# Optimization experiments

Measured on AMD Instinct MI355X. Metric: run time of the kernel, lower is better.

The kernel has to match this reference:

```python
import jax, jax.numpy as jnp
import numpy as np

N_NODES = 100000
N_EDGES = 1600000
IN_CH = 128
OUT_CH = 64
HID = 2 * OUT_CH  # 128


def setup_inputs() -> dict:
    key = jax.random.key(0)
    ks = jax.random.split(key, 8)
    s = lambda fan_in: 1.0 / np.sqrt(fan_in)
    return {
        "x": jax.random.normal(ks[0], (N_NODES, IN_CH), jnp.float32),
        "edge_index": jax.random.randint(ks[1], (2, N_EDGES), 0, N_NODES, dtype=jnp.int32),
        "W1": jax.random.normal(ks[2], (IN_CH, HID), jnp.float32) * s(IN_CH),
        "b1": jnp.zeros((HID,), jnp.float32),
        "W2": jax.random.normal(ks[3], (HID, HID), jnp.float32) * s(HID),
        "b2": jnp.zeros((HID,), jnp.float32),
        "W3": jax.random.normal(ks[4], (HID, OUT_CH), jnp.float32) * s(HID),
        "b3": jnp.zeros((OUT_CH,), jnp.float32),
    }


def reference(x, edge_index, W1, b1, W2, b2, W3, b3):
    N = x.shape[0]
    # GCNConv (PyG semantics): add self-loops, symmetric deg^{-1/2} normalization,
    # linear transform, scatter-add aggregation at destination, then bias.
    loops = jnp.arange(N, dtype=edge_index.dtype)
    src = jnp.concatenate([edge_index[0], loops])  # [E+N]
    dst = jnp.concatenate([edge_index[1], loops])  # [E+N]
    deg = jnp.zeros((N,), x.dtype).at[dst].add(1.0)  # in-degree incl. self-loop
    dinv = jnp.where(deg > 0, jax.lax.rsqrt(deg), 0.0)
    norm = (dinv[src] * dinv[dst])[:, None]  # [E+N, 1]

    def gcn_conv(h, W, b):
        h = h @ W  # transform first (smaller when out < in)
        msg = h[src] * norm  # gather + normalize, [E+N, C]
        agg = jnp.zeros((N, h.shape[1]), h.dtype).at[dst].add(msg)  # scatter-add
        return agg + b

    h = jax.nn.relu(gcn_conv(x, W1, b1))
    h = jax.nn.relu(gcn_conv(h, W2, b2))
    h = gcn_conv(h, W3, b3)
    return jnp.min(h, axis=0)  # min-pool over nodes -> [OUT_CH]
```

## Files before the change

kernel.cpp:

```cpp
#include <hip/hip_runtime.h>
#include <stdint.h>
#include <stddef.h>
#include <float.h>

typedef short bf16x8 __attribute__((ext_vector_type(8)));
typedef float f32x4 __attribute__((ext_vector_type(4)));

static __device__ __forceinline__ unsigned enc_min(float v) {
  unsigned u = __float_as_uint(v);
  return (u & 0x80000000u) ? ~u : (u | 0x80000000u);
}
static __device__ __forceinline__ unsigned short f2bf(float f) {
  unsigned u = __float_as_uint(f);
  u += 0x7fffu + ((u >> 16) & 1u);
  return (unsigned short)(u >> 16);
}
static __device__ __forceinline__ float bf2f(unsigned short b) {
  return __uint_as_float(((unsigned)b) << 16);
}
static __device__ __forceinline__ void acc8(float* a, uint4 v) {
  a[0] += __uint_as_float(v.x << 16);
  a[1] += __uint_as_float(v.x & 0xffff0000u);
  a[2] += __uint_as_float(v.y << 16);
  a[3] += __uint_as_float(v.y & 0xffff0000u);
  a[4] += __uint_as_float(v.z << 16);
  a[5] += __uint_as_float(v.z & 0xffff0000u);
  a[6] += __uint_as_float(v.w << 16);
  a[7] += __uint_as_float(v.w & 0xffff0000u);
}

__global__ __launch_bounds__(256) void k_count_bin(const int* __restrict__ edge, int E, int N,
                                                   int* __restrict__ cnt8,
                                                   int* __restrict__ bin_cur,
                                                   int2* __restrict__ pairs,
                                                   int binw, int bcap) {
  __shared__ int h[8], gbase[8], lfill[8];
  int cslot = blockIdx.x & 7;
  int* cnt = cnt8 + (size_t)cslot * N;
  int tid = threadIdx.x;
  int nt = (E + 1023) >> 10;
  for (int t = blockIdx.x; t < nt; t += gridDim.x) {
    int e0 = t << 10;
    if (tid < 8) { h[tid] = 0; lfill[tid] = 0; }
    __syncthreads();
    int d[4], s[4], g[4], r[4];
#pragma unroll
    for (int k = 0; k < 4; ++k) {
      int e = e0 + tid + k * 256;
      d[k] = -1;
      if (e < E) {
        d[k] = edge[E + e];
        s[k] = edge[e];
        g[k] = (int)((unsigned)d[k] / (unsigned)binw);
        r[k] = atomicAdd(&cnt[d[k]], 1);
        atomicAdd(&h[g[k]], 1);
      }
    }
    __syncthreads();
    if (tid < 8) gbase[tid] = atomicAdd(&bin_cur[tid], h[tid]);
    __syncthreads();
#pragma unroll
    for (int k = 0; k < 4; ++k) {
      if (d[k] >= 0) {
        int rr = atomicAdd(&lfill[g[k]], 1);
        int p = gbase[g[k]] + rr;
        unsigned packed = (unsigned)d[k] | ((unsigned)cslot << 17) | ((unsigned)r[k] << 20);
        if (p < bcap) pairs[(size_t)g[k] * bcap + p] = make_int2((int)packed, s[k]);
      }
    }
    __syncthreads();
  }
}

__global__ void k_scan1(const int* __restrict__ cnt8, int N,
                        int* __restrict__ cnt, int* __restrict__ incl,
                        int* __restrict__ bsum) {
  __shared__ int sm[1024];
  int tid = threadIdx.x;
  int i = blockIdx.x * 1024 + tid;
  int v = 0;
  if (i < N) {
#pragma unroll
    for (int g = 0; g < 8; ++g) v += cnt8[(size_t)g * N + i];
    cnt[i] = v;
  }
  sm[tid] = v;
  __syncthreads();
  for (int off = 1; off < 1024; off <<= 1) {
    int t = (tid >= off) ? sm[tid - off] : 0;
    __syncthreads();
    sm[tid] += t;
    __syncthreads();
  }
  if (i < N) incl[i] = sm[tid];
  if (tid == 1023) bsum[blockIdx.x] = sm[1023];
}

__global__ void k_scan2(const int* __restrict__ bsum, int nb, int* __restrict__ boff) {
  __shared__ int sm[128];
  int tid = threadIdx.x;
  int v = (tid < nb) ? bsum[tid] : 0;
  sm[tid] = v;
  __syncthreads();
  for (int off = 1; off < 128; off <<= 1) {
    int t = (tid >= off) ? sm[tid - off] : 0;
    __syncthreads();
    sm[tid] += t;
    __syncthreads();
  }
  if (tid < nb) boff[tid] = sm[tid] - v;
}

__global__ void k_aux(const int* __restrict__ cnt, const int* __restrict__ cnt8,
                      const int* __restrict__ incl, const int* __restrict__ boff,
                      int N, int E, int* __restrict__ row_ptr,
                      int* __restrict__ base8, float* __restrict__ dinv) {
  int i = blockIdx.x * blockDim.x + threadIdx.x;
  if (i < N) {
    int rp = incl[i] - cnt[i] + boff[i >> 10];
    row_ptr[i] = rp;
    dinv[i] = 1.0f / sqrtf((float)(cnt[i] + 1));
    int run = rp;
#pragma unroll
    for (int c = 0; c < 8; ++c) {
      base8[(size_t)c * N + i] = run;
      run += cnt8[(size_t)c * N + i];
    }
  } else if (i == N) {
    row_ptr[N] = E;
  }
}

__global__ void k_prepw(const float* __restrict__ W1, const float* __restrict__ W2,
                        const float* __restrict__ W3,
                        unsigned short* __restrict__ w1h, unsigned short* __restrict__ w1l,
                        unsigned short* __restrict__ w2h, unsigned short* __restrict__ w2l,
                        unsigned short* __restrict__ w3h, unsigned short* __restrict__ w3l) {
  const int K = 128;
  int idx = blockIdx.x * 256 + threadIdx.x;
  const float* W;
  unsigned short *oh, *ol;
  int Nn, base;
  if (idx < 16384) { W = W1; Nn = 128; oh = w1h; ol = w1l; base = idx; }
  else if (idx < 32768) { W = W2; Nn = 128; oh = w2h; ol = w2l; base = idx - 16384; }
  else if (idx < 40960) { W = W3; Nn = 64; oh = w3h; ol = w3l; base = idx - 32768; }
  else return;
  int n = base / K, k = base % K;
  float w = W[(size_t)k * Nn + n];
  unsigned short h = f2bf(w);
  unsigned short l = f2bf(w - bf2f(h));
  int nf = n >> 4, mloc = n & 15, kci = k >> 5, quad = (k >> 3) & 3, j = k & 7;
  size_t o = ((size_t)((nf * 4 + kci) * 64 + quad * 16 + mloc)) * 8 + j;
  oh[o] = h;
  ol[o] = l;
}

template <int NFW>
static __device__ __forceinline__ void gemm_body(const float* __restrict__ A,
                                                 const unsigned short* __restrict__ Wfh,
                                                 const unsigned short* __restrict__ Wfl,
                                                 const float* __restrict__ dinv,
                                                 unsigned short* __restrict__ P, int M,
                                                 int blk) {
  const int K = 128;
  const int COUT = NFW * 64;
  __shared__ unsigned short Ah[64][136];
  __shared__ unsigned short Al[64][136];
  int tid = threadIdx.x;
  int m0 = blk * 64;
  int w = tid >> 6, lane = tid & 63;

  bf16x8 bh[NFW][4], bl[NFW][4];
#pragma unroll
  for (int i = 0; i < NFW; ++i)
#pragma unroll
    for (int kci = 0; kci < 4; ++kci) {
      size_t o = ((size_t)(((w * NFW + i) * 4 + kci) * 64 + lane)) * 8;
      bh[i][kci] = *(const bf16x8*)&Wfh[o];
      bl[i][kci] = *(const bf16x8*)&Wfl[o];
    }

#pragma unroll
  for (int q = 0; q < 8; ++q) {
    int f = q * 256 + tid;
    int m = f >> 5, k4 = f & 31;
    int row = m0 + m;
    if (row >= M) row = M - 1;
    float4 v = *(const float4*)&A[(size_t)row * K + k4 * 4];
    unsigned short h0 = f2bf(v.x), h1 = f2bf(v.y), h2 = f2bf(v.z), h3 = f2bf(v.w);
    unsigned short l0 = f2bf(v.x - bf2f(h0)), l1 = f2bf(v.y - bf2f(h1));
    unsigned short l2 = f2bf(v.z - bf2f(h2)), l3 = f2bf(v.w - bf2f(h3));
    uint2 hh, ll;
    hh.x = (unsigned)h0 | ((unsigned)h1 << 16);
    hh.y = (unsigned)h2 | ((unsigned)h3 << 16);
    ll.x = (unsigned)l0 | ((unsigned)l1 << 16);
    ll.y = (unsigned)l2 | ((unsigned)l3 << 16);
    *(uint2*)&Ah[m][k4 * 4] = hh;
    *(uint2*)&Al[m][k4 * 4] = ll;
  }
  __syncthreads();

  int mloc = lane & 15, quad = lane >> 4;
  f32x4 acc[4][NFW];
#pragma unroll
  for (int rt = 0; rt < 4; ++rt)
#pragma unroll
    for (int i = 0; i < NFW; ++i) acc[rt][i] = (f32x4){0.f, 0.f, 0.f, 0.f};

#pragma unroll
  for (int rt = 0; rt < 4; ++rt) {
    const unsigned short* ph = &Ah[rt * 16 + mloc][quad * 8];
    const unsigned short* pl = &Al[rt * 16 + mloc][quad * 8];
#pragma unroll
    for (int kci = 0; kci < 4; ++kci) {
      bf16x8 ah = *(const bf16x8*)(ph + kci * 32);
      bf16x8 al = *(const bf16x8*)(pl + kci * 32);
#pragma unroll
      for (int i = 0; i < NFW; ++i) {
        acc[rt][i] = __builtin_amdgcn_mfma_f32_16x16x32_bf16(al, bh[i][kci], acc[rt][i], 0, 0, 0);
        acc[rt][i] = __builtin_amdgcn_mfma_f32_16x16x32_bf16(ah, bl[i][kci], acc[rt][i], 0, 0, 0);
        acc[rt][i] = __builtin_amdgcn_mfma_f32_16x16x32_bf16(ah, bh[i][kci], acc[rt][i], 0, 0, 0);
      }
    }
  }

#pragma unroll
  for (int rt = 0; rt < 4; ++rt) {
    int rbase = m0 + rt * 16 + quad * 4;
#pragma unroll
    for (int r = 0; r < 4; ++r) {
      int row = rbase + r;
      if (row < M) {
        float dv = dinv[row];
#pragma unroll
        for (int i = 0; i < NFW; ++i) {
          int nf = w * NFW + i;
          P[(size_t)row * COUT + nf * 16 + mloc] = f2bf(acc[rt][i][r] * dv);
        }
      }
    }
  }
}

__global__ __launch_bounds__(256) void k_fill_gemm(const float* __restrict__ A,
                                                   const unsigned short* __restrict__ Wfh,
                                                   const unsigned short* __restrict__ Wfl,
                                                   const float* __restrict__ dinv,
                                                   unsigned short* __restrict__ P, int M,
                                                   const int2* __restrict__ pairs,
                                                   const int* __restrict__ bin_cur, int bcap,
                                                   const int* __restrict__ base8, int N,
                                                   int* __restrict__ srcs, int ns) {
  if ((int)blockIdx.x >= ns) {
    gemm_body<2>(A, Wfh, Wfl, dinv, P, M, blockIdx.x - ns);
  } else {
    int grp = blockIdx.x & 7;
    int bslot = blockIdx.x >> 3;
    int nslot = ns >> 3;
    int cnt_g = bin_cur[grp];
    if (cnt_g > bcap) cnt_g = bcap;
    const int2* pp = pairs + (size_t)grp * bcap;
    for (int i = bslot * blockDim.x + threadIdx.x; i < cnt_g; i += nslot * blockDim.x) {
      int2 pr = pp[i];
      unsigned w = (unsigned)pr.x;
      int d = (int)(w & 0x1FFFFu);
      int c = (int)((w >> 17) & 7u);
      int r = (int)(w >> 20);
      srcs[base8[(size_t)c * N + d] + r] = pr.y;
    }
  }
}

template <int NFW>
__global__ __launch_bounds__(256) void k_agg_gemm(const unsigned short* __restrict__ Pin,
                                                  const int* __restrict__ row_ptr,
                                                  const int* __restrict__ srcs,
                                                  const float* __restrict__ dinv,
                                                  const float* __restrict__ bias,
                                                  const unsigned short* __restrict__ Wfh,
                                                  const unsigned short* __restrict__ Wfl,
                                                  unsigned short* __restrict__ Pout, int N) {
  const int COUT = NFW * 64;
  __shared__ unsigned short Ah[16][136];
  __shared__ unsigned short Al[16][136];
  int tid = threadIdx.x;
  int wv = tid >> 6, lane = tid & 63;
  int grp = lane >> 4, sub = lane & 15;
  int m = wv * 4 + grp;
  int d = blockIdx.x * 16 + m;
  int dc = d < N ? d : N - 1;
  bool valid = d < N;
  unsigned soff = (unsigned)sub * 16u;
  const char* Pb = (const char*)Pin;

  float a[8] = {0.f, 0.f, 0.f, 0.f, 0.f, 0.f, 0.f, 0.f};
  {
    uint4 v = *(const uint4*)(Pb + ((unsigned)dc * 256u + soff));
    acc8(a, v);
  }
  int lo = row_ptr[dc];
  int hi = row_ptr[valid ? d + 1 : dc];
  int j = lo;
  for (; j + 4 <= hi; j += 4) {
    unsigned i0 = (unsigned)srcs[j];
    unsigned i1 = (unsigned)srcs[j + 1];
    unsigned i2 = (unsigned)srcs[j + 2];
    unsigned i3 = (unsigned)srcs[j + 3];
    uint4 v0 = *(const uint4*)(Pb + (i0 * 256u + soff));
    uint4 v1 = *(const uint4*)(Pb + (i1 * 256u + soff));
    uint4 v2 = *(const uint4*)(Pb + (i2 * 256u + soff));
    uint4 v3 = *(const uint4*)(Pb + (i3 * 256u + soff));
    acc8(a, v0);
    acc8(a, v1);
    acc8(a, v2);
    acc8(a, v3);
  }
  for (; j < hi; ++j) {
    unsigned i0 = (unsigned)srcs[j];
    uint4 v0 = *(const uint4*)(Pb + (i0 * 256u + soff));
    acc8(a, v0);
  }

  bf16x8 bh[NFW][4], bl[NFW][4];
#pragma unroll
  for (int i = 0; i < NFW; ++i)
#pragma unroll
    for (int kci = 0; kci < 4; ++kci) {
      size_t o = ((size_t)(((wv * NFW + i) * 4 + kci) * 64 + lane)) * 8;
      bh[i][kci] = *(const bf16x8*)&Wfh[o];
      bl[i][kci] = *(const bf16x8*)&Wfl[o];
    }

  float dv = dinv[dc];
  int ch0 = sub * 8;
  float4 bv0 = *(const float4*)&bias[ch0];
  float4 bv1 = *(const float4*)&bias[ch0 + 4];
  float h[8];
  h[0] = dv * a[0] + bv0.x; h[1] = dv * a[1] + bv0.y;
  h[2] = dv * a[2] + bv0.z; h[3] = dv * a[3] + bv0.w;
  h[4] = dv * a[4] + bv1.x; h[5] = dv * a[5] + bv1.y;
  h[6] = dv * a[6] + bv1.z; h[7] = dv * a[7] + bv1.w;
#pragma unroll
  for (int k = 0; k < 8; ++k) h[k] = fmaxf(h[k], 0.f);
  unsigned short hb[8], lb[8];
#pragma unroll
  for (int k = 0; k < 8; ++k) {
    hb[k] = f2bf(h[k]);
    lb[k] = f2bf(h[k] - bf2f(hb[k]));
  }
  uint4 HH, LL;
  HH.x = (unsigned)hb[0] | ((unsigned)hb[1] << 16);
  HH.y = (unsigned)hb[2] | ((unsigned)hb[3] << 16);
  HH.z = (unsigned)hb[4] | ((unsigned)hb[5] << 16);
  HH.w = (unsigned)hb[6] | ((unsigned)hb[7] << 16);
  LL.x = (unsigned)lb[0] | ((unsigned)lb[1] << 16);
  LL.y = (unsigned)lb[2] | ((unsigned)lb[3] << 16);
  LL.z = (unsigned)lb[4] | ((unsigned)lb[5] << 16);
  LL.w = (unsigned)lb[6] | ((unsigned)lb[7] << 16);
  *(uint4*)&Ah[m][ch0] = HH;
  *(uint4*)&Al[m][ch0] = LL;
  __syncthreads();

  int mloc = lane & 15, quad = lane >> 4;
  f32x4 acc[NFW];
#pragma unroll
  for (int i = 0; i < NFW; ++i) acc[i] = (f32x4){0.f, 0.f, 0.f, 0.f};
#pragma unroll
  for (int kci = 0; kci < 4; ++kci) {
    bf16x8 ah = *(const bf16x8*)&Ah[mloc][quad * 8 + kci * 32];
    bf16x8 al = *(const bf16x8*)&Al[mloc][quad * 8 + kci * 32];
#pragma unroll
    for (int i = 0; i < NFW; ++i) {
      acc[i] = __builtin_amdgcn_mfma_f32_16x16x32_bf16(al, bh[i][kci], acc[i], 0, 0, 0);
      acc[i] = __builtin_amdgcn_mfma_f32_16x16x32_bf16(ah, bl[i][kci], acc[i], 0, 0, 0);
      acc[i] = __builtin_amdgcn_mfma_f32_16x16x32_bf16(ah, bh[i][kci], acc[i], 0, 0, 0);
    }
  }
  int rbase = blockIdx.x * 16 + quad * 4;
#pragma unroll
  for (int r = 0; r < 4; ++r) {
    int row = rbase + r;
    if (row < N) {
      float dvr = dinv[row];
#pragma unroll
      for (int i = 0; i < NFW; ++i) {
        int nf = wv * NFW + i;
        Pout[(size_t)row * COUT + nf * 16 + mloc] = f2bf(acc[i][r] * dvr);
      }
    }
  }
}

__global__ __launch_bounds__(256) void k_agg_pool(const unsigned short* __restrict__ P,
                                                  const int* __restrict__ row_ptr,
                                                  const int* __restrict__ srcs,
                                                  const float* __restrict__ dinv,
                                                  const float* __restrict__ bias,
                                                  unsigned* __restrict__ minenc, int N) {
  const int CAP = 448;
  __shared__ int s_idx[4][CAP];
  __shared__ float s_red[4][32];
  int tid = threadIdx.x;
  int wv = tid >> 6, lane = tid & 63;
  int b8 = blockIdx.x & 7;
  int slice = b8 >> 2, part = b8 & 3;
  int g0 = ((blockIdx.x >> 3) * 4 + part) * 64 + wv * 16;
  const char* Pb = (const char*)P + slice * 64;

  int i = lane >> 2, q = lane & 3;
  unsigned qoff = (unsigned)q * 16u;
  int d = g0 + i;
  int dc = d < N ? d : N - 1;
  bool valid = d < N;

  int e0 = row_ptr[g0 < N ? g0 : N];
  int e1 = row_ptr[(g0 + 16) < N ? (g0 + 16) : N];
  int lo_n = row_ptr[dc];
  int hi_n = row_ptr[valid ? d + 1 : dc];

  float a[8];
  {
    uint4 v = *(const uint4*)(Pb + ((unsigned)dc * 128u + qoff));
    a[0] = __uint_as_float(v.x << 16);
    a[1] = __uint_as_float(v.x & 0xffff0000u);
    a[2] = __uint_as_float(v.y << 16);
    a[3] = __uint_as_float(v.y & 0xffff0000u);
    a[4] = __uint_as_float(v.z << 16);
    a[5] = __uint_as_float(v.z & 0xffff0000u);
    a[6] = __uint_as_float(v.w << 16);
    a[7] = __uint_as_float(v.w & 0xffff0000u);
  }

  for (int w0 = e0; w0 < e1; w0 += CAP) {
    int wend = min(w0 + CAP, e1);
    int cnt = wend - w0;
    __builtin_amdgcn_wave_barrier();
    for (int t = lane; t < cnt; t += 64) s_idx[wv][t] = srcs[w0 + t];
    __builtin_amdgcn_wave_barrier();
    int j = max(lo_n, w0), hi = min(hi_n, wend);
    for (; j + 4 <= hi; j += 4) {
      unsigned i0 = (unsigned)s_idx[wv][j - w0];
      unsigned i1 = (unsigned)s_idx[wv][j - w0 + 1];
      unsigned i2 = (unsigned)s_idx[wv][j - w0 + 2];
      unsigned i3 = (unsigned)s_idx[wv][j - w0 + 3];
      uint4 v0 = *(const uint4*)(Pb + (i0 * 128u + qoff));
      uint4 v1 = *(const uint4*)(Pb + (i1 * 128u + qoff));
      uint4 v2 = *(const uint4*)(Pb + (i2 * 128u + qoff));
      uint4 v3 = *(const uint4*)(Pb + (i3 * 128u + qoff));
      acc8(a, v0);
      acc8(a, v1);
      acc8(a, v2);
      acc8(a, v3);
    }
    for (; j < hi; ++j) {
      unsigned i0 = (unsigned)s_idx[wv][j - w0];
      uint4 v0 = *(const uint4*)(Pb + (i0 * 128u + qoff));
      acc8(a, v0);
    }
  }

  int c0 = slice * 32 + q * 8;
  float dv = dinv[dc];
  float4 bv0 = *(const float4*)&bias[c0];
  float4 bv1 = *(const float4*)&bias[c0 + 4];
  float h[8];
  h[0] = dv * a[0] + bv0.x; h[1] = dv * a[1] + bv0.y;
  h[2] = dv * a[2] + bv0.z; h[3] = dv * a[3] + bv0.w;
  h[4] = dv * a[4] + bv1.x; h[5] = dv * a[5] + bv1.y;
  h[6] = dv * a[6] + bv1.z; h[7] = dv * a[7] + bv1.w;

  if (!valid) {
#pragma unroll
    for (int k = 0; k < 8; ++k) h[k] = FLT_MAX;
  }
#pragma unroll
  for (int off = 4; off < 64; off <<= 1) {
#pragma unroll
    for (int k = 0; k < 8; ++k) h[k] = fminf(h[k], __shfl_xor(h[k], off, 64));
  }
  if (lane < 4) {
#pragma unroll
    for (int k = 0; k < 8; ++k) s_red[wv][q * 8 + k] = h[k];
  }
  __syncthreads();
  if (tid < 32) {
    float mn = fminf(fminf(s_red[0][tid], s_red[1][tid]),
                     fminf(s_red[2][tid], s_red[3][tid]));
    atomicMin(&minenc[slice * 32 + tid], enc_min(mn));
  }
}

__global__ void k_decode(const unsigned* __restrict__ minenc, float* __restrict__ out) {
  int c = threadIdx.x;
  unsigned k = minenc[c];
  unsigned u = (k & 0x80000000u) ? (k & 0x7FFFFFFFu) : ~k;
  out[c] = __uint_as_float(u);
}

extern "C" void kernel_launch(void* const* d_in, const int* in_sizes, int n_in,
                              void* d_out, int out_size, void* d_ws, size_t ws_size,
                              hipStream_t stream) {
  const float* X  = (const float*)d_in[0];
  const int* edge = (const int*)d_in[1];
  const float* W1 = (const float*)d_in[2];
  const float* b1 = (const float*)d_in[3];
  const float* W2 = (const float*)d_in[4];
  const float* b2 = (const float*)d_in[5];
  const float* W3 = (const float*)d_in[6];
  const float* b3 = (const float*)d_in[7];
  float* out = (float*)d_out;

  const int IN_CH = 128;
  int N = in_sizes[0] / IN_CH;
  int E = in_sizes[1] / 2;

  char* ws = (char*)d_ws;
  size_t off = 0;
  auto alloc = [&](size_t bytes) {
    void* p = ws + off;
    off = (off + bytes + 255) & ~(size_t)255;
    return p;
  };
  unsigned short* P1 = (unsigned short*)alloc((size_t)N * 128 * 2);
  unsigned short* P2 = (unsigned short*)alloc((size_t)N * 128 * 2);
  int* srcs      = (int*)alloc((size_t)E * 4);
  int* cnt8      = (int*)alloc((size_t)8 * N * 4);
  int* base8     = (int*)alloc((size_t)8 * N * 4);
  int* cnt       = (int*)alloc((size_t)N * 4);
  int* incl      = (int*)alloc((size_t)N * 4);
  int* row_ptr   = (int*)alloc((size_t)(N + 1) * 4);
  float* dinv    = (float*)alloc((size_t)N * 4);
  int* bsum      = (int*)alloc(1024);
  int* boff      = (int*)alloc(1024);
  int* bin_cur   = (int*)alloc(256);
  unsigned* minenc = (unsigned*)alloc(256);
  unsigned short* w1h = (unsigned short*)alloc(16384 * 2);
  unsigned short* w1l = (unsigned short*)alloc(16384 * 2);
  unsigned short* w2h = (unsigned short*)alloc(16384 * 2);
  unsigned short* w2l = (unsigned short*)alloc(16384 * 2);
  unsigned short* w3h = (unsigned short*)alloc(8192 * 2);
  unsigned short* w3l = (unsigned short*)alloc(8192 * 2);

  int bcap = E / 8 + 65536;
  int binw = (N + 7) / 8;
  int2* pairs = (int2*)P2;
  unsigned short* P3 = P1;

  hipMemsetAsync(cnt8, 0, (size_t)8 * N * 4, stream);
  hipMemsetAsync(bin_cur, 0, 32, stream);
  hipMemsetAsync(minenc, 0xFF, 64 * 4, stream);

  int nb = (N + 1023) / 1024;
  int gx = (N + 63) / 64;
  int ns = 1024;
  int gagg = (N + 15) / 16;
  int c64 = (N + 255) / 256;
  k_prepw<<<160, 256, 0, stream>>>(W1, W2, W3, w1h, w1l, w2h, w2l, w3h, w3l);
  k_count_bin<<<782, 256, 0, stream>>>(edge, E, N, cnt8, bin_cur, pairs, binw, bcap);
  k_scan1<<<nb, 1024, 0, stream>>>(cnt8, N, cnt, incl, bsum);
  k_scan2<<<1, 128, 0, stream>>>(bsum, nb, boff);
  k_aux<<<(N + 256) / 256, 256, 0, stream>>>(cnt, cnt8, incl, boff, N, E, row_ptr, base8, dinv);

  k_fill_gemm<<<ns + gx, 256, 0, stream>>>(X, w1h, w1l, dinv, P1, N,
                                           pairs, bin_cur, bcap, base8, N, srcs, ns);
  k_agg_gemm<2><<<gagg, 256, 0, stream>>>(P1, row_ptr, srcs, dinv, b1, w2h, w2l, P2, N);
  k_agg_gemm<1><<<gagg, 256, 0, stream>>>(P2, row_ptr, srcs, dinv, b2, w3h, w3l, P3, N);
  k_agg_pool<<<c64 * 8, 256, 0, stream>>>(P3, row_ptr, srcs, dinv, b3, minenc, N);
  k_decode<<<1, 64, 0, stream>>>(minenc, out);
}
```

Baseline: 420.6 us.

## Split fused aggregate+GEMM into sliced aggregation and separate MFMA GEMM kernels

Changes the GEMM output layout to channel-sliced blocks of 16 bf16 columns per slice, so each aggregation block gathers 32-byte rows from a compact slice that is more likely to stay in cache. The fused aggregate-then-GEMM kernels are unfocused into separate aggregation kernels that write fp32 H, followed by standalone MFMA GEMM kernels. This is meant to improve gather locality, since the per-slice working set is much smaller than full 256-byte rows. In exchange it adds a round trip of a 51 MB fp32 intermediate through memory per layer and extra kernel launches. It also switches srcs loads to nontemporal hints.

```diff
diff --git a/kernel.cpp b/kernel.cpp
--- a/kernel.cpp
+++ b/kernel.cpp
@@ -163,7 +163,6 @@
                                                  unsigned short* __restrict__ P, int M,
                                                  int blk) {
   const int K = 128;
-  const int COUT = NFW * 64;
   __shared__ unsigned short Ah[64][136];
   __shared__ unsigned short Al[64][136];
   int tid = threadIdx.x;
@@ -235,11 +234,20 @@
 #pragma unroll
         for (int i = 0; i < NFW; ++i) {
           int nf = w * NFW + i;
-          P[(size_t)row * COUT + nf * 16 + mloc] = f2bf(acc[rt][i][r] * dv);
+          P[(size_t)nf * M * 16 + (size_t)row * 16 + mloc] = f2bf(acc[rt][i][r] * dv);
         }
       }
     }
   }
+}
+
+template <int NFW>
+__global__ __launch_bounds__(256) void k_gemm_mfma(const float* __restrict__ A,
+                                                   const unsigned short* __restrict__ Wfh,
+                                                   const unsigned short* __restrict__ Wfl,
+                                                   const float* __restrict__ dinv,
+                                                   unsigned short* __restrict__ P, int M) {
+  gemm_body<NFW>(A, Wfh, Wfl, dinv, P, M, blockIdx.x);
 }
 
 __global__ __launch_bounds__(256) void k_fill_gemm(const float* __restrict__ A,
@@ -271,68 +279,116 @@
   }
 }
 
-template <int NFW>
-__global__ __launch_bounds__(256) void k_agg_gemm(const unsigned short* __restrict__ Pin,
-                                                  const int* __restrict__ row_ptr,
-                                                  const int* __restrict__ srcs,
-                                                  const float* __restrict__ dinv,
-                                                  const float* __restrict__ bias,
-                                                  const unsigned short* __restrict__ Wfh,
-                                                  const unsigned short* __restrict__ Wfl,
-                                                  unsigned short* __restrict__ Pout, int N) {
-  const int COUT = NFW * 64;
-  __shared__ unsigned short Ah[16][136];
-  __shared__ unsigned short Al[16][136];
+__global__ __launch_bounds__(256) void k_agg_sl(const unsigned short* __restrict__ Pin,
+                                                const int* __restrict__ row_ptr,
+                                                const int* __restrict__ srcs,
+                                                const float* __restrict__ dinv,
+                                                const float* __restrict__ bias,
+                                                float* __restrict__ H, int N) {
   int tid = threadIdx.x;
   int wv = tid >> 6, lane = tid & 63;
-  int grp = lane >> 4, sub = lane & 15;
-  int m = wv * 4 + grp;
-  int d = blockIdx.x * 16 + m;
-  int dc = d < N ? d : N - 1;
-  bool valid = d < N;
-  unsigned soff = (unsigned)sub * 16u;
-  const char* Pb = (const char*)Pin;
+  int slice = blockIdx.x & 7;
+  int part = blockIdx.x >> 3;
+  int pd = lane >> 1, q = lane & 1;
+  int d = part * 128 + wv * 32 + pd;
+  if (d >= N) return;
+  const char* Pb = (const char*)Pin + (size_t)slice * N * 32;
+  unsigned qoff = (unsigned)q * 16u;
 
   float a[8] = {0.f, 0.f, 0.f, 0.f, 0.f, 0.f, 0.f, 0.f};
   {
-    uint4 v = *(const uint4*)(Pb + ((unsigned)dc * 256u + soff));
+    uint4 v = *(const uint4*)(Pb + ((unsigned)d * 32u + qoff));
     acc8(a, v);
   }
-  int lo = row_ptr[dc];
-  int hi = row_ptr[valid ? d + 1 : dc];
+  int lo = row_ptr[d];
+  int hi = row_ptr[d + 1];
   int j = lo;
   for (; j + 4 <= hi; j += 4) {
-    unsigned i0 = (unsigned)srcs[j];
-    unsigned i1 = (unsigned)srcs[j + 1];
-    unsigned i2 = (unsigned)srcs[j + 2];
-    unsigned i3 = (unsigned)srcs[j + 3];
-    uint4 v0 = *(const uint4*)(Pb + (i0 * 256u + soff));
-    uint4 v1 = *(const uint4*)(Pb + (i1 * 256u + soff));
-    uint4 v2 = *(const uint4*)(Pb + (i2 * 256u + soff));
-    uint4 v3 = *(const uint4*)(Pb + (i3 * 256u + soff));
+    unsigned i0 = (unsigned)__builtin_nontemporal_load(&srcs[j]);
+    unsigned i1 = (unsigned)__builtin_nontemporal_load(&srcs[j + 1]);
+    unsigned i2 = (unsigned)__builtin_nontemporal_load(&srcs[j + 2]);
+    unsigned i3 = (unsigned)__builtin_nontemporal_load(&srcs[j + 3]);
+    uint4 v0 = *(const uint4*)(Pb + (i0 * 32u + qoff));
+    uint4 v1 = *(const uint4*)(Pb + (i1 * 32u + qoff));
+    uint4 v2 = *(const uint4*)(Pb + (i2 * 32u + qoff));
+    uint4 v3 = *(const uint4*)(Pb + (i3 * 32u + qoff));
     acc8(a, v0);
     acc8(a, v1);
     acc8(a, v2);
     acc8(a, v3);
   }
   for (; j < hi; ++j) {
-    unsigned i0 = (unsigned)srcs[j];
-    uint4 v0 = *(const uint4*)(Pb + (i0 * 256u + soff));
+    unsigned i0 = (unsigned)__builtin_nontemporal_load(&srcs[j]);
+    uint4 v0 = *(const uint4*)(Pb + (i0 * 32u + qoff));
     acc8(a, v0);
   }
 
-  bf16x8 bh[NFW][4], bl[NFW][4];
-#pragma unroll
-  for (int i = 0; i < NFW; ++i)
-#pragma unroll
-    for (int kci = 0; kci < 4; ++kci) {
-      size_t o = ((size_t)(((wv * NFW + i) * 4 + kci) * 64 + lane)) * 8;
-      bh[i][kci] = *(const bf16x8*)&Wfh[o];
-      bl[i][kci] = *(const bf16x8*)&Wfl[o];
-    }
+  float dv = dinv[d];
+  int ch0 = slice * 16 + q * 8;
+  float4 bv0 = *(const float4*)&bias[ch0];
+  float4 bv1 = *(const float4*)&bias[ch0 + 4];
+  float4 o0, o1;
+  o0.x = fmaxf(dv * a[0] + bv0.x, 0.f);
+  o0.y = fmaxf(dv * a[1] + bv0.y, 0.f);
+  o0.z = fmaxf(dv * a[2] + bv0.z, 0.f);
+  o0.w = fmaxf(dv * a[3] + bv0.w, 0.f);
+  o1.x = fmaxf(dv * a[4] + bv1.x, 0.f);
+  o1.y = fmaxf(dv * a[5] + bv1.y, 0.f);
+  o1.z = fmaxf(dv * a[6] + bv1.z, 0.f);
+  o1.w = fmaxf(dv * a[7] + bv1.w, 0.f);
+  *(float4*)&H[(size_t)d * 128 + ch0] = o0;
+  *(float4*)&H[(size_t)d * 128 + ch0 + 4] = o1;
+}
+
+__global__ __launch_bounds__(256) void k_pool_sl(const unsigned short* __restrict__ Pin,
+                                                 const int* __restrict__ row_ptr,
+                                                 const int* __restrict__ srcs,
+                                                 const float* __restrict__ dinv,
+                                                 const float* __restrict__ bias,
+                                                 unsigned* __restrict__ minenc, int N) {
+  __shared__ float s_red[4][16];
+  int tid = threadIdx.x;
+  int wv = tid >> 6, lane = tid & 63;
+  int slice = blockIdx.x & 3;
+  int part = blockIdx.x >> 2;
+  int pd = lane >> 1, q = lane & 1;
+  int d = part * 128 + wv * 32 + pd;
+  bool valid = d < N;
+  int dc = valid ? d : N - 1;
+  const char* Pb = (const char*)Pin + (size_t)slice * N * 32;
+  unsigned qoff = (unsigned)q * 16u;
+
+  float a[8] = {0.f, 0.f, 0.f, 0.f, 0.f, 0.f, 0.f, 0.f};
+  int lo = 0, hi = 0;
+  if (valid) {
+    uint4 v = *(const uint4*)(Pb + ((unsigned)d * 32u + qoff));
+    acc8(a, v);
+    lo = row_ptr[d];
+    hi = row_ptr[d + 1];
+  }
+  int j = lo;
+  for (; j + 4 <= hi; j += 4) {
+    unsigned i0 = (unsigned)__builtin_nontemporal_load(&srcs[j]);
+    unsigned i1 = (unsigned)__builtin_nontemporal_load(&srcs[j + 1]);
+    unsigned i2 = (unsigned)__builtin_nontemporal_load(&srcs[j + 2]);
+    unsigned i3 = (unsigned)__builtin_nontemporal_load(&srcs[j + 3]);
+    uint4 v0 = *(const uint4*)(Pb + (i0 * 32u + qoff));
+    uint4 v1 = *(const uint4*)(Pb + (i1 * 32u + qoff));
+    uint4 v2 = *(const uint4*)(Pb + (i2 * 32u + qoff));
+    uint4 v3 = *(const uint4*)(Pb + (i3 * 32u + qoff));
+    acc8(a, v0);
+    acc8(a, v1);
+    acc8(a, v2);
+    acc8(a, v3);
+  }
+  for (; j < hi; ++j) {
+    unsigned i0 = (unsigned)__builtin_nontemporal_load(&srcs[j]);
+    uint4 v0 = *(const uint4*)(Pb + (i0 * 32u + qoff));
+    acc8(a, v0);
+  }
 
   float dv = dinv[dc];
-  int ch0 = sub * 8;
+  int ch0 = slice * 16 + q * 8;
   float4 bv0 = *(const float4*)&bias[ch0];
   float4 bv1 = *(const float4*)&bias[ch0 + 4];
   float h[8];
@@ -340,153 +396,24 @@
   h[2] = dv * a[2] + bv0.z; h[3] = dv * a[3] + bv0.w;
   h[4] = dv * a[4] + bv1.x; h[5] = dv * a[5] + bv1.y;
   h[6] = dv * a[6] + bv1.z; h[7] = dv * a[7] + bv1.w;
-#pragma unroll
-  for (int k = 0; k < 8; ++k) h[k] = fmaxf(h[k], 0.f);
-  unsigned short hb[8], lb[8];
-#pragma unroll
-  for (int k = 0; k < 8; ++k) {
-    hb[k] = f2bf(h[k]);
-    lb[k] = f2bf(h[k] - bf2f(hb[k]));
-  }
-  uint4 HH, LL;
-  HH.x = (unsigned)hb[0] | ((unsigned)hb[1] << 16);
-  HH.y = (unsigned)hb[2] | ((unsigned)hb[3] << 16);
-  HH.z = (unsigned)hb[4] | ((unsigned)hb[5] << 16);
-  HH.w = (unsigned)hb[6] | ((unsigned)hb[7] << 16);
-  LL.x = (unsigned)lb[0] | ((unsigned)lb[1] << 16);
-  LL.y = (unsigned)lb[2] | ((unsigned)lb[3] << 16);
-  LL.z = (unsigned)lb[4] | ((unsigned)lb[5] << 16);
-  LL.w = (unsigned)lb[6] | ((unsigned)lb[7] << 16);
-  *(uint4*)&Ah[m][ch0] = HH;
-  *(uint4*)&Al[m][ch0] = LL;
+  if (!valid) {
+#pragma unroll
+    for (int k = 0; k < 8; ++k) h[k] = FLT_MAX;
+  }
+#pragma unroll
+  for (int off = 2; off < 64; off <<= 1) {
+#pragma unroll
+    for (int k = 0; k < 8; ++k) h[k] = fminf(h[k], __shfl_xor(h[k], off, 64));
+  }
+  if (pd == 0) {
+#pragma unroll
+    for (int k = 0; k < 8; ++k) s_red[wv][q * 8 + k] = h[k];
+  }
   __syncthreads();
-
-  int mloc = lane & 15, quad = lane >> 4;
-  f32x4 acc[NFW];
-#pragma unroll
-  for (int i = 0; i < NFW; ++i) acc[i] = (f32x4){0.f, 0.f, 0.f, 0.f};
-#pragma unroll
-  for (int kci = 0; kci < 4; ++kci) {
-    bf16x8 ah = *(const bf16x8*)&Ah[mloc][quad * 8 + kci * 32];
-    bf16x8 al = *(const bf16x8*)&Al[mloc][quad * 8 + kci * 32];
-#pragma unroll
-    for (int i = 0; i < NFW; ++i) {
-      acc[i] = __builtin_amdgcn_mfma_f32_16x16x32_bf16(al, bh[i][kci], acc[i], 0, 0, 0);
-      acc[i] = __builtin_amdgcn_mfma_f32_16x16x32_bf16(ah, bl[i][kci], acc[i], 0, 0, 0);
-      acc[i] = __builtin_amdgcn_mfma_f32_16x16x32_bf16(ah, bh[i][kci], acc[i], 0, 0, 0);
-    }
-  }
-  int rbase = blockIdx.x * 16 + quad * 4;
-#pragma unroll
-  for (int r = 0; r < 4; ++r) {
-    int row = rbase + r;
-    if (row < N) {
-      float dvr = dinv[row];
-#pragma unroll
-      for (int i = 0; i < NFW; ++i) {
-        int nf = wv * NFW + i;
-        Pout[(size_t)row * COUT + nf * 16 + mloc] = f2bf(acc[i][r] * dvr);
-      }
-    }
-  }
-}
-
-__global__ __launch_bounds__(256) void k_agg_pool(const unsigned short* __restrict__ P,
-                                                  const int* __restrict__ row_ptr,
-                                                  const int* __restrict__ srcs,
-                                                  const float* __restrict__ dinv,
-                                                  const float* __restrict__ bias,
-                                                  unsigned* __restrict__ minenc, int N) {
-  const int CAP = 448;
-  __shared__ int s_idx[4][CAP];
-  __shared__ float s_red[4][32];
-  int tid = threadIdx.x;
-  int wv = tid >> 6, lane = tid & 63;
-  int b8 = blockIdx.x & 7;
-  int slice = b8 >> 2, part = b8 & 3;
-  int g0 = ((blockIdx.x >> 3) * 4 + part) * 64 + wv * 16;
-  const char* Pb = (const char*)P + slice * 64;
-
-  int i = lane >> 2, q = lane & 3;
-  unsigned qoff = (unsigned)q * 16u;
-  int d = g0 + i;
-  int dc = d < N ? d : N - 1;
-  bool valid = d < N;
-
-  int e0 = row_ptr[g0 < N ? g0 : N];
-  int e1 = row_ptr[(g0 + 16) < N ? (g0 + 16) : N];
-  int lo_n = row_ptr[dc];
-  int hi_n = row_ptr[valid ? d + 1 : dc];
-
-  float a[8];
-  {
-    uint4 v = *(const uint4*)(Pb + ((unsigned)dc * 128u + qoff));
-    a[0] = __uint_as_float(v.x << 16);
-    a[1] = __uint_as_float(v.x & 0xffff0000u);
-    a[2] = __uint_as_float(v.y << 16);
-    a[3] = __uint_as_float(v.y & 0xffff0000u);
-    a[4] = __uint_as_float(v.z << 16);
-    a[5] = __uint_as_float(v.z & 0xffff0000u);
-    a[6] = __uint_as_float(v.w << 16);
-    a[7] = __uint_as_float(v.w & 0xffff0000u);
-  }
-
-  for (int w0 = e0; w0 < e1; w0 += CAP) {
-    int wend = min(w0 + CAP, e1);
-    int cnt = wend - w0;
-    __builtin_amdgcn_wave_barrier();
-    for (int t = lane; t < cnt; t += 64) s_idx[wv][t] = srcs[w0 + t];
-    __builtin_amdgcn_wave_barrier();
-    int j = max(lo_n, w0), hi = min(hi_n, wend);
-    for (; j + 4 <= hi; j += 4) {
-      unsigned i0 = (unsigned)s_idx[wv][j - w0];
-      unsigned i1 = (unsigned)s_idx[wv][j - w0 + 1];
-      unsigned i2 = (unsigned)s_idx[wv][j - w0 + 2];
-      unsigned i3 = (unsigned)s_idx[wv][j - w0 + 3];
-      uint4 v0 = *(const uint4*)(Pb + (i0 * 128u + qoff));
-      uint4 v1 = *(const uint4*)(Pb + (i1 * 128u + qoff));
-      uint4 v2 = *(const uint4*)(Pb + (i2 * 128u + qoff));
-      uint4 v3 = *(const uint4*)(Pb + (i3 * 128u + qoff));
-      acc8(a, v0);
-      acc8(a, v1);
-      acc8(a, v2);
-      acc8(a, v3);
-    }
-    for (; j < hi; ++j) {
-      unsigned i0 = (unsigned)s_idx[wv][j - w0];
-      uint4 v0 = *(const uint4*)(Pb + (i0 * 128u + qoff));
-      acc8(a, v0);
-    }
-  }
-
-  int c0 = slice * 32 + q * 8;
-  float dv = dinv[dc];
-  float4 bv0 = *(const float4*)&bias[c0];
-  float4 bv1 = *(const float4*)&bias[c0 + 4];
-  float h[8];
-  h[0] = dv * a[0] + bv0.x; h[1] = dv * a[1] + bv0.y;
-  h[2] = dv * a[2] + bv0.z; h[3] = dv * a[3] + bv0.w;
-  h[4] = dv * a[4] + bv1.x; h[5] = dv * a[5] + bv1.y;
-  h[6] = dv * a[6] + bv1.z; h[7] = dv * a[7] + bv1.w;
-
-  if (!valid) {
-#pragma unroll
-    for (int k = 0; k < 8; ++k) h[k] = FLT_MAX;
-  }
-#pragma unroll
-  for (int off = 4; off < 64; off <<= 1) {
-#pragma unroll
-    for (int k = 0; k < 8; ++k) h[k] = fminf(h[k], __shfl_xor(h[k], off, 64));
-  }
-  if (lane < 4) {
-#pragma unroll
-    for (int k = 0; k < 8; ++k) s_red[wv][q * 8 + k] = h[k];
-  }
-  __syncthreads();
-  if (tid < 32) {
+  if (tid < 16) {
     float mn = fminf(fminf(s_red[0][tid], s_red[1][tid]),
                      fminf(s_red[2][tid], s_red[3][tid]));
-    atomicMin(&minenc[slice * 32 + tid], enc_min(mn));
+    atomicMin(&minenc[slice * 16 + tid], enc_min(mn));
   }
 }
 
@@ -523,6 +450,7 @@
   };
   unsigned short* P1 = (unsigned short*)alloc((size_t)N * 128 * 2);
   unsigned short* P2 = (unsigned short*)alloc((size_t)N * 128 * 2);
+  float* H       = (float*)alloc((size_t)N * 128 * 4);
   int* srcs      = (int*)alloc((size_t)E * 4);
   int* cnt8      = (int*)alloc((size_t)8 * N * 4);
   int* base8     = (int*)alloc((size_t)8 * N * 4);
@@ -553,8 +481,7 @@
   int nb = (N + 1023) / 1024;
   int gx = (N + 63) / 64;
   int ns = 1024;
-  int gagg = (N + 15) / 16;
-  int c64 = (N + 255) / 256;
+  int parts = (N + 127) / 128;
   k_prepw<<<160, 256, 0, stream>>>(W1, W2, W3, w1h, w1l, w2h, w2l, w3h, w3l);
   k_count_bin<<<782, 256, 0, stream>>>(edge, E, N, cnt8, bin_cur, pairs, binw, bcap);
   k_scan1<<<nb, 1024, 0, stream>>>(cnt8, N, cnt, incl, bsum);
@@ -563,8 +490,10 @@
 
   k_fill_gemm<<<ns + gx, 256, 0, stream>>>(X, w1h, w1l, dinv, P1, N,
                                            pairs, bin_cur, bcap, base8, N, srcs, ns);
-  k_agg_gemm<2><<<gagg, 256, 0, stream>>>(P1, row_ptr, srcs, dinv, b1, w2h, w2l, P2, N);
-  k_agg_gemm<1><<<gagg, 256, 0, stream>>>(P2, row_ptr, srcs, dinv, b2, w3h, w3l, P3, N);
-  k_agg_pool<<<c64 * 8, 256, 0, stream>>>(P3, row_ptr, srcs, dinv, b3, minenc, N);
+  k_agg_sl<<<parts * 8, 256, 0, stream>>>(P1, row_ptr, srcs, dinv, b1, H, N);
+  k_gemm_mfma<2><<<gx, 256, 0, stream>>>(H, w2h, w2l, dinv, P2, N);
+  k_agg_sl<<<parts * 8, 256, 0, stream>>>(P2, row_ptr, srcs, dinv, b2, H, N);
+  k_gemm_mfma<1><<<gx, 256, 0, stream>>>(H, w3h, w3l, dinv, P3, N);
+  k_pool_sl<<<parts * 4, 256, 0, stream>>>(P3, row_ptr, srcs, dinv, b3, minenc, N);
   k_decode<<<1, 64, 0, stream>>>(minenc, out);
 }
```

New measurement: 628.7 us. 49.5% more time.
